# Performance work log

Hardware: AMD Instinct MI355X
Metric: run time of the kernel (lower is better)

The kernel has to match this reference:

```python
import jax, jax.numpy as jnp
from jax import lax
import numpy as np

B, C, H, W = 8, 256, 128, 128
MID, RMID = C // 2, C // 4          # heatmap-head mid, radius-head mid channels
K = 5                                # K_max centers
THR = 0.1                            # nms_threshold
SMIN, SMAX = 0.05, 0.45              # sigma clamp
BETA = 1.5                           # prior aspect ratio sigma_y/sigma_x
DMAX = 0.08                          # sigma residual max
RMIN, RMAX = 0.03, 0.40              # radius range
BNEPS = 1e-5
PI = float(np.pi)


def setup_inputs() -> dict:
    key = jax.random.key(0)
    ks = jax.random.split(key, 12)
    def n(k, shp, s):
        return jax.random.normal(k, shp, dtype=jnp.float32) * s
    return {
        'x': n(ks[0], (B, C, H, W), 1.0),
        # heatmap head: DWConv3x3 -> PW1x1 -> BN/ReLU -> Conv3x3 -> BN/ReLU -> Conv1x1(+bias=-2) -> Sigmoid
        'hm_dw': n(ks[1], (C, 1, 3, 3), 0.1),
        'hm_pw1': n(ks[2], (MID, C, 1, 1), 0.05),
        'hm_g1': jnp.ones((MID,), jnp.float32), 'hm_b1': jnp.zeros((MID,), jnp.float32),
        'hm_c3': n(ks[3], (MID, MID, 3, 3), 0.05),
        'hm_g2': jnp.ones((MID,), jnp.float32), 'hm_b2': jnp.zeros((MID,), jnp.float32),
        'hm_out_w': n(ks[4], (1, MID, 1, 1), 0.2), 'hm_out_b': jnp.full((1,), -2.0, jnp.float32),
        # radius head: DWConv3x3 -> PW1x1 -> BN/ReLU -> Conv1x1(+bias) -> Sigmoid -> [r_min, r_max]
        'r_dw': n(ks[5], (C, 1, 3, 3), 0.1),
        'r_pw1': n(ks[6], (RMID, C, 1, 1), 0.05),
        'r_g': jnp.ones((RMID,), jnp.float32), 'r_b': jnp.zeros((RMID,), jnp.float32),
        'r_out_w': n(ks[7], (1, RMID, 1, 1), 0.1), 'r_out_b': jnp.zeros((1,), jnp.float32),
        # per-center param predictor
        'log_alpha': jnp.zeros((1,), jnp.float32),
        'mlp_w1': n(ks[8], (C, C // 2), 0.05), 'mlp_b1': jnp.zeros((C // 2,), jnp.float32),
        'mlp_w2': n(ks[9], (C // 2, 4), 0.05), 'mlp_b2': jnp.zeros((4,), jnp.float32),
    }


def conv(x, w, groups=1, pad=0):
    return lax.conv_general_dilated(x, w, (1, 1), [(pad, pad), (pad, pad)],
                                    dimension_numbers=('NCHW', 'OIHW', 'NCHW'),
                                    feature_group_count=groups)


def bn(x, g, b):
    # eval-mode BatchNorm with running_mean=0, running_var=1
    s = g / np.sqrt(1.0 + BNEPS)
    return x * s[:, None, None] + b[:, None, None]


def bilinear_sample(fm, cx, cy):
    # fm: (C,H,W); cx,cy: (K,) normalized in [-1,1]; align_corners=True, border padding
    px = jnp.clip((cx + 1.0) * 0.5 * (W - 1), 0.0, W - 1)
    py = jnp.clip((cy + 1.0) * 0.5 * (H - 1), 0.0, H - 1)
    x0 = jnp.floor(px).astype(jnp.int32); x1 = jnp.minimum(x0 + 1, W - 1)
    y0 = jnp.floor(py).astype(jnp.int32); y1 = jnp.minimum(y0 + 1, H - 1)
    wx = px - x0; wy = py - y0
    v00 = fm[:, y0, x0]; v01 = fm[:, y0, x1]
    v10 = fm[:, y1, x0]; v11 = fm[:, y1, x1]          # (C,K)
    v = (1 - wy) * ((1 - wx) * v00 + wx * v01) + wy * ((1 - wx) * v10 + wx * v11)
    return v.T                                          # (K,C)


def reference(x, hm_dw, hm_pw1, hm_g1, hm_b1, hm_c3, hm_g2, hm_b2, hm_out_w, hm_out_b,
              r_dw, r_pw1, r_g, r_b, r_out_w, r_out_b,
              log_alpha, mlp_w1, mlp_b1, mlp_w2, mlp_b2):
    relu = jax.nn.relu
    # ---- heatmap head ----
    h = conv(x, hm_dw, groups=C, pad=1)
    h = conv(h, hm_pw1)
    h = relu(bn(h, hm_g1, hm_b1))
    h = conv(h, hm_c3, pad=1)
    h = relu(bn(h, hm_g2, hm_b2))
    heat = jax.nn.sigmoid(conv(h, hm_out_w) + hm_out_b[None, :, None, None])  # (B,1,H,W)
    # ---- MaxPool NMS + topk center extraction ----
    pooled = lax.reduce_window(heat, -jnp.inf, lax.max, (1, 1, 3, 3), (1, 1, 1, 1), 'SAME')
    peaks = (heat * (pooled == heat).astype(heat.dtype)).reshape(B, H * W)
    top_vals, top_idx = lax.top_k(peaks, K)             # (B,K)
    valid = (top_vals >= THR).astype(jnp.float32)
    row = (top_idx // W).astype(jnp.float32)
    col = (top_idx % W).astype(jnp.float32)
    ny = 2.0 * row / (H - 1) - 1.0
    nx = 2.0 * col / (W - 1) - 1.0
    centers = lax.stop_gradient(jnp.stack([nx, ny], -1) * valid[..., None])  # (B,K,2)
    # ---- radius map ----
    r = conv(x, r_dw, groups=C, pad=1)
    r = conv(r, r_pw1)
    r = relu(bn(r, r_g, r_b))
    rmap = RMIN + jax.nn.sigmoid(conv(r, r_out_w) + r_out_b[None, :, None, None]) * (RMAX - RMIN)
    # ---- per-center feature/radius sampling + param MLP ----
    cx, cy = centers[..., 0], centers[..., 1]
    feat = jax.vmap(bilinear_sample)(x, cx, cy)          # (B,K,C)
    r_k = jax.vmap(bilinear_sample)(rmap, cx, cy)[..., 0]  # (B,K)
    alpha = jax.nn.softplus(log_alpha)[0]
    p = relu(feat @ mlp_w1 + mlp_b1) @ mlp_w2 + mlp_b2   # (B,K,4)
    dsx = jnp.tanh(p[..., 0]) * DMAX
    dsy = jnp.tanh(p[..., 1]) * DMAX
    theta = jnp.tanh(p[..., 2]) * PI
    wgt = jax.nn.sigmoid(p[..., 3])
    sx = jnp.clip(alpha * r_k + dsx, SMIN, SMAX)
    sy = jnp.clip(alpha * r_k * BETA + dsy, SMIN, SMAX)
    # ---- rotated Gaussian mixture render ----
    yy = jnp.linspace(-1.0, 1.0, H)
    xx = jnp.linspace(-1.0, 1.0, W)
    gy, gx = jnp.meshgrid(yy, xx, indexing='ij')         # (H,W)
    dx = gx[None, None] - cx[..., None, None]            # (B,K,H,W)
    dy = gy[None, None] - cy[..., None, None]
    ct = jnp.cos(theta)[..., None, None]
    st = jnp.sin(theta)[..., None, None]
    xr = ct * dx + st * dy
    yr = -st * dx + ct * dy
    sx4 = sx[..., None, None]; sy4 = sy[..., None, None]
    G = jnp.exp(-(xr ** 2 / (2.0 * sx4 ** 2 + 1e-6) + yr ** 2 / (2.0 * sy4 ** 2 + 1e-6)))
    m = valid[..., None, None]
    mw = wgt[..., None, None] * m                         # (B,K,1,1)
    wsum = jnp.maximum(mw.sum(axis=1, keepdims=True), 1e-6)
    mix = (G * (mw / wsum) * m).sum(axis=1, keepdims=True)  # (B,1,H,W)
    attn = jax.nn.sigmoid(mix * 4.0 - 2.0)
    return jnp.concatenate([attn, heat], axis=1)          # (B,2,H,W)
```

## Files before the change

### kernel.cpp

```cpp
#include <hip/hip_runtime.h>
#include <hip/hip_bf16.h>
#include <math.h>

typedef __hip_bfloat16 bf16;
using short8 = __attribute__((ext_vector_type(8))) short;
using f32x4  = __attribute__((ext_vector_type(4))) float;

#define NB 8
#define NC 256
#define NH 128
#define NW 128
#define NHW 16384
#define MID 128
#define HP 130
#define HPP (HP*HP)

__device__ __forceinline__ float b2f(bf16 v){ return __bfloat162float(v); }
__device__ __forceinline__ bf16 f2b(float v){ return __float2bfloat16(v); }
#define BN_S 0.9999950000374997f

__global__ __launch_bounds__(256) void k_cvt(const float* __restrict__ src, bf16* __restrict__ dst, int n){
  int i = blockIdx.x*256 + threadIdx.x;
  if(i < n) dst[i] = f2b(src[i]);
}

__global__ __launch_bounds__(256) void k_trans(const float* __restrict__ src, bf16* __restrict__ dst){
  int i = blockIdx.x*256 + threadIdx.x;
  if(i >= MID*MID*9) return;
  int tau = i % 9; int c = (i/9) % MID; int m = i/(9*MID);
  dst[((size_t)tau*MID + m)*MID + c] = f2b(src[i]);
}

__global__ __launch_bounds__(256) void k_zero(bf16* __restrict__ h1p){
  int s = blockIdx.x*256 + threadIdx.x;
  const int NPLANE = NB*16;
  const int PER = 2*HP + 2*(HP-2);
  if(s >= NPLANE*PER) return;
  int plane = s / PER, j = s % PER;
  int px;
  if(j < HP)            px = j;
  else if(j < 2*HP)     px = 129*HP + (j - HP);
  else if(j < 2*HP+128) px = (j - 2*HP + 1)*HP;
  else                  px = (j - (2*HP+128) + 1)*HP + 129;
  short8 z = {0,0,0,0,0,0,0,0};
  *(short8*)((ushort*)h1p + ((size_t)plane*HPP + px)*8) = z;
}

__global__ __launch_bounds__(256) void k_dwb(const float* __restrict__ x,
                                             const float* __restrict__ w9,
                                             bf16* __restrict__ outB8){
  __shared__ float tile[8][10][136];
  int tid = threadIdx.x;
  int cg = blockIdx.y, b = blockIdx.z;
  int y0 = blockIdx.x*8;
  #pragma unroll
  for(int it=0; it<10; it++){
    int idx = it*256 + tid;
    int c = idx / 320, rem = idx % 320;
    int row = rem >> 5, col4 = rem & 31;
    int gy = y0 - 1 + row;
    float4 v = make_float4(0.f,0.f,0.f,0.f);
    if(gy >= 0 && gy < NH)
      v = *(const float4*)(x + ((size_t)(b*NC + cg*8 + c))*NHW + gy*NW + col4*4);
    *(float4*)&tile[c][row][4 + col4*4] = v;
  }
  if(tid < 160){
    int c = tid/20, rem = tid%20;
    int row = rem>>1;
    tile[c][row][(rem&1) ? 132 : 3] = 0.f;
  }
  __syncthreads();
  int row = tid >> 5;
  int t   = tid & 31;
  union { ushort u[8]; short8 v; } o[4];
  for(int c=0;c<8;c++){
    float wf[9];
    #pragma unroll
    for(int i=0;i<9;i++) wf[i] = w9[(cg*8+c)*9 + i];
    float a0=0.f, a1=0.f, a2=0.f, a3=0.f;
    #pragma unroll
    for(int dr=0;dr<3;dr++){
      float f0 = tile[c][row+dr][3 + 4*t];
      float4 v4 = *(const float4*)&tile[c][row+dr][4 + 4*t];
      float f5 = tile[c][row+dr][8 + 4*t];
      float w0 = wf[dr*3+0], w1 = wf[dr*3+1], w2 = wf[dr*3+2];
      a0 += f0*w0   + v4.x*w1 + v4.y*w2;
      a1 += v4.x*w0 + v4.y*w1 + v4.z*w2;
      a2 += v4.y*w0 + v4.z*w1 + v4.w*w2;
      a3 += v4.z*w0 + v4.w*w1 + f5*w2;
    }
    bf16 q0=f2b(a0), q1=f2b(a1), q2=f2b(a2), q3=f2b(a3);
    o[0].u[c]=*(ushort*)&q0; o[1].u[c]=*(ushort*)&q1;
    o[2].u[c]=*(ushort*)&q2; o[3].u[c]=*(ushort*)&q3;
  }
  size_t base = ((size_t)(b*32+cg))*NHW + (y0+row)*NW + 4*t;
  #pragma unroll
  for(int i=0;i<4;i++) *(short8*)(outB8 + (base+i)*8) = o[i].v;
}

template<int MT, int MODE>
__global__ __launch_bounds__(256) void k_pw(const bf16* __restrict__ in8,
                                            const bf16* __restrict__ wA,
                                            const float* __restrict__ g,
                                            const float* __restrict__ bias,
                                            const float* __restrict__ hw,
                                            const float* __restrict__ hb,
                                            bf16*  __restrict__ h1p,
                                            float* __restrict__ outMap){
  int tid = threadIdx.x;
  int bidx = blockIdx.x;
  int b = bidx >> 8;
  int p0 = (bidx & 255)*64;
  int lane = tid & 63, wave = tid >> 6;
  int n = lane & 15, quad = lane >> 4;
  size_t pix = p0 + wave*16 + n;
  const ushort* inU = (const ushort*)in8;
  const ushort* wU  = (const ushort*)wA;

  f32x4 acc[MT];
  #pragma unroll
  for(int i=0;i<MT;i++){
    #pragma unroll
    for(int r=0;r<4;r++) acc[i][r] = 0.f;
  }
  #pragma unroll
  for(int k0=0;k0<NC;k0+=32){
    short8 bfrag = *(const short8*)&inU[ (((size_t)(b*32) + (k0>>3) + quad)*NHW + pix)*8 ];
    #pragma unroll
    for(int mt=0;mt<MT;mt++){
      short8 afrag = *(const short8*)&wU[(size_t)(mt*16 + n)*NC + k0 + quad*8];
      acc[mt] = __builtin_amdgcn_mfma_f32_16x16x32_bf16(afrag, bfrag, acc[mt], 0, 0, 0);
    }
  }

  if(MODE == 0){
    int py = ((int)(pix>>7) + 1)*HP + (int)(pix&127) + 1;
    #pragma unroll
    for(int mt=0;mt<MT;mt++){
      int mg  = mt*2 + (quad>>1);
      int off = (quad&1)*4;
      union { ushort u[4]; ushort4 v; } t;
      #pragma unroll
      for(int r=0;r<4;r++){
        int m = mt*16 + quad*4 + r;
        float v = acc[mt][r]*(g[m]*BN_S) + bias[m];
        bf16 ab = f2b(fmaxf(v, 0.f));
        t.u[r] = *(ushort*)&ab;
      }
      *(ushort4*)((ushort*)h1p + (((size_t)(b*16+mg))*HPP + py)*8 + off) = t.v;
    }
  }else{
    float ph = 0.f;
    #pragma unroll
    for(int mt=0;mt<MT;mt++){
      #pragma unroll
      for(int r=0;r<4;r++){
        int m = mt*16 + quad*4 + r;
        float v = acc[mt][r]*(g[m]*BN_S) + bias[m];
        ph += fmaxf(v, 0.f) * hw[m];
      }
    }
    ph += __shfl_xor(ph, 16);
    ph += __shfl_xor(ph, 32);
    if(lane < 16){
      float sg = 1.f/(1.f + expf(-(ph + hb[0])));
      outMap[(size_t)b*NHW + pix] = 0.03f + sg*0.37f;
    }
  }
}

__global__ __launch_bounds__(256) void k_c3(const bf16* __restrict__ h1p,
                                            const bf16* __restrict__ wT,
                                            const float* __restrict__ g,
                                            const float* __restrict__ bias,
                                            const float* __restrict__ hw,
                                            const float* __restrict__ hb,
                                            float* __restrict__ heatF,
                                            float* __restrict__ out){
  int tid = threadIdx.x;
  int y = blockIdx.x, b = blockIdx.y;
  int lane = tid & 63, wave = tid >> 6;
  int n = lane & 15, quad = lane >> 4;
  const ushort* inU = (const ushort*)h1p;
  const ushort* wU  = (const ushort*)wT;
  f32x4 acc[8][2];
  #pragma unroll
  for(int i=0;i<8;i++){
    #pragma unroll
    for(int j=0;j<2;j++){
      #pragma unroll
      for(int r=0;r<4;r++) acc[i][j][r] = 0.f;
    }
  }
  int colbase = wave*32 + n;
  for(int dy=0;dy<3;dy++){
    #pragma unroll
    for(int dx=0;dx<3;dx++){
      const ushort* wtb = wU + (size_t)(dy*3+dx)*MID*MID;
      #pragma unroll
      for(int k0=0;k0<MID;k0+=32){
        size_t base = ((size_t)(b*16) + (k0>>3) + quad)*HPP + (size_t)(y+dy)*HP + colbase + dx;
        short8 b0 = *(const short8*)&inU[base*8];
        short8 b1 = *(const short8*)&inU[(base+16)*8];
        #pragma unroll
        for(int mt=0;mt<8;mt++){
          short8 a = *(const short8*)&wtb[(size_t)(mt*16 + n)*MID + k0 + quad*8];
          acc[mt][0] = __builtin_amdgcn_mfma_f32_16x16x32_bf16(a, b0, acc[mt][0], 0, 0, 0);
          acc[mt][1] = __builtin_amdgcn_mfma_f32_16x16x32_bf16(a, b1, acc[mt][1], 0, 0, 0);
        }
      }
    }
  }
  #pragma unroll
  for(int ng=0;ng<2;ng++){
    float ph = 0.f;
    #pragma unroll
    for(int mt=0;mt<8;mt++){
      #pragma unroll
      for(int r=0;r<4;r++){
        int m = mt*16 + quad*4 + r;
        float v = acc[mt][ng][r]*(g[m]*BN_S) + bias[m];
        ph += fmaxf(v, 0.f) * hw[m];
      }
    }
    ph += __shfl_xor(ph, 16);
    ph += __shfl_xor(ph, 32);
    if(lane < 16){
      int pix = y*NW + wave*32 + ng*16 + lane;
      float sg = 1.f/(1.f + expf(-(ph + hb[0])));
      heatF[(size_t)b*NHW + pix] = sg;
      out[((size_t)(b*2+1))*NHW + pix] = sg;
    }
  }
}

__global__ __launch_bounds__(256) void k_topk1(const float* __restrict__ heat,
                                               float* __restrict__ sv_g,
                                               int*   __restrict__ si_g){
  __shared__ float sv[256*5];
  __shared__ int   si[256*5];
  int blk = blockIdx.x, b = blockIdx.y, tid = threadIdx.x;
  const float* hb = heat + (size_t)b*NHW;
  float tv[5]; int ti[5];
  #pragma unroll
  for(int i=0;i<5;i++){ tv[i] = -1.f; ti[i] = 0x7fffffff; }
  for(int s=0;s<2;s++){
    int p = blk*512 + s*256 + tid;
    int y = p >> 7, x = p & 127;
    float v = hb[p];
    float mx = v;
    for(int dy=-1;dy<=1;dy++){
      int yy = y+dy; if(yy<0||yy>=NH) continue;
      for(int dx=-1;dx<=1;dx++){
        int xc = x+dx; if(xc<0||xc>=NW) continue;
        mx = fmaxf(mx, hb[yy*NW+xc]);
      }
    }
    float pv = (v == mx) ? v : 0.f;
    #pragma unroll
    for(int j=0;j<5;j++){
      if(pv > tv[j] || (pv == tv[j] && p < ti[j])){
        for(int q=4;q>j;q--){ tv[q]=tv[q-1]; ti[q]=ti[q-1]; }
        tv[j] = pv; ti[j] = p;
        break;
      }
    }
  }
  #pragma unroll
  for(int i=0;i<5;i++){ sv[tid*5+i] = tv[i]; si[tid*5+i] = ti[i]; }
  __syncthreads();
  if(tid < 64){
    float mv[5]; int mi[5];
    #pragma unroll
    for(int i=0;i<5;i++){ mv[i] = -1.f; mi[i] = 0x7fffffff; }
    for(int s=0;s<4;s++){
      int t2 = tid + s*64;
      for(int i=0;i<5;i++){
        float pv = sv[t2*5+i]; int pi = si[t2*5+i];
        for(int j=0;j<5;j++){
          if(pv > mv[j] || (pv == mv[j] && pi < mi[j])){
            for(int q=4;q>j;q--){ mv[q]=mv[q-1]; mi[q]=mi[q-1]; }
            mv[j] = pv; mi[j] = pi;
            break;
          }
        }
      }
    }
    for(int i=0;i<5;i++){ sv[tid*5+i] = mv[i]; si[tid*5+i] = mi[i]; }
  }
  __syncthreads();
  if(tid == 0){
    float fv[5]; int fi[5];
    #pragma unroll
    for(int i=0;i<5;i++){ fv[i] = -1.f; fi[i] = 0x7fffffff; }
    for(int t2=0;t2<64;t2++){
      for(int i=0;i<5;i++){
        float pv = sv[t2*5+i]; int pi = si[t2*5+i];
        for(int j=0;j<5;j++){
          if(pv > fv[j] || (pv == fv[j] && pi < fi[j])){
            for(int q=4;q>j;q--){ fv[q]=fv[q-1]; fi[q]=fi[q-1]; }
            fv[j] = pv; fi[j] = pi;
            break;
          }
        }
      }
    }
    for(int i=0;i<5;i++){
      sv_g[(b*32 + blk)*5 + i] = fv[i];
      si_g[(b*32 + blk)*5 + i] = fi[i];
    }
  }
}

__global__ __launch_bounds__(256) void k_topk2(const float* __restrict__ sv_g,
                                               const int*   __restrict__ si_g,
                                               float* __restrict__ centers){
  __shared__ float cv[160];
  __shared__ int   ci[160];
  int b = blockIdx.x, tid = threadIdx.x;
  if(tid < 160){ cv[tid] = sv_g[b*160 + tid]; ci[tid] = si_g[b*160 + tid]; }
  __syncthreads();
  if(tid < 160){
    float v = cv[tid]; int idx = ci[tid];
    int rank = 0;
    for(int j=0;j<160;j++){
      float vj = cv[j]; int ij = ci[j];
      rank += (vj > v || (vj == v && ij < idx)) ? 1 : 0;
    }
    if(rank < 5){
      float valid = (v >= 0.1f) ? 1.f : 0.f;
      float row = (float)(idx >> 7);
      float col = (float)(idx & 127);
      float ny = 2.f*row/127.f - 1.f;
      float nx = 2.f*col/127.f - 1.f;
      float* cp = centers + (b*5+rank)*4;
      cp[0] = nx*valid; cp[1] = ny*valid; cp[2] = v; cp[3] = valid;
    }
  }
}

__global__ __launch_bounds__(256) void k_params(const float* __restrict__ x,
                                                const float* __restrict__ rmap,
                                                const float* __restrict__ centers,
                                                const float* __restrict__ w1,
                                                const float* __restrict__ b1,
                                                const float* __restrict__ w2,
                                                const float* __restrict__ b2,
                                                const float* __restrict__ log_alpha,
                                                float* __restrict__ params){
  __shared__ float feat[NC];
  __shared__ float hmid[128];
  __shared__ float pp[4];
  int bk = blockIdx.x;
  int b = bk/5;
  int tid = threadIdx.x;
  float cx = centers[bk*4+0];
  float cy = centers[bk*4+1];
  float valid = centers[bk*4+3];
  float px = fminf(fmaxf((cx+1.f)*0.5f*(NW-1), 0.f), (float)(NW-1));
  float py = fminf(fmaxf((cy+1.f)*0.5f*(NH-1), 0.f), (float)(NH-1));
  int x0 = (int)floorf(px); int x1 = min(x0+1, NW-1);
  int y0 = (int)floorf(py); int y1 = min(y0+1, NH-1);
  float wx = px - (float)x0, wy = py - (float)y0;
  {
    const float* xb = x + ((size_t)b*NC + tid)*NHW;
    float v00 = xb[y0*NW+x0], v01 = xb[y0*NW+x1];
    float v10 = xb[y1*NW+x0], v11 = xb[y1*NW+x1];
    feat[tid] = (1.f-wy)*((1.f-wx)*v00 + wx*v01) + wy*((1.f-wx)*v10 + wx*v11);
  }
  __syncthreads();
  if(tid < 128){
    float a = b1[tid];
    for(int c=0;c<NC;c++) a += feat[c]*w1[c*128+tid];
    hmid[tid] = fmaxf(a, 0.f);
  }
  __syncthreads();
  if(tid < 4){
    float a = b2[tid];
    for(int j=0;j<128;j++) a += hmid[j]*w2[j*4+tid];
    pp[tid] = a;
  }
  __syncthreads();
  if(tid == 0){
    const float* rb = rmap + (size_t)b*NHW;
    float r00 = rb[y0*NW+x0], r01 = rb[y0*NW+x1];
    float r10 = rb[y1*NW+x0], r11 = rb[y1*NW+x1];
    float rk = (1.f-wy)*((1.f-wx)*r00 + wx*r01) + wy*((1.f-wx)*r10 + wx*r11);
    float la = log_alpha[0];
    float alpha = logf(1.f + expf(la));
    float dsx = tanhf(pp[0])*0.08f;
    float dsy = tanhf(pp[1])*0.08f;
    float theta = tanhf(pp[2])*3.14159265358979323846f;
    float wgt = 1.f/(1.f + expf(-pp[3]));
    float sx = fminf(fmaxf(alpha*rk + dsx, 0.05f), 0.45f);
    float sy = fminf(fmaxf(alpha*rk*1.5f + dsy, 0.05f), 0.45f);
    float* P = params + bk*8;
    P[0] = cx; P[1] = cy;
    P[2] = cosf(theta); P[3] = sinf(theta);
    P[4] = 1.f/(2.f*sx*sx + 1e-6f);
    P[5] = 1.f/(2.f*sy*sy + 1e-6f);
    P[6] = wgt*valid; P[7] = valid;
  }
}

__global__ __launch_bounds__(256) void k_attn(const float* __restrict__ params,
                                              float* __restrict__ out){
  int tid = threadIdx.x;
  int p = blockIdx.x*256 + tid;
  int b = blockIdx.y;
  int y = p >> 7, x = p & 127;
  float gx = -1.f + 2.f*(float)x/127.f;
  float gy = -1.f + 2.f*(float)y/127.f;
  const float* Pb = params + b*40;
  float wsum = 0.f;
  #pragma unroll
  for(int k=0;k<5;k++) wsum += Pb[k*8+6];
  wsum = fmaxf(wsum, 1e-6f);
  float mix = 0.f;
  #pragma unroll
  for(int k=0;k<5;k++){
    const float* P = Pb + k*8;
    float dx = gx - P[0], dy = gy - P[1];
    float xr =  P[2]*dx + P[3]*dy;
    float yr = -P[3]*dx + P[2]*dy;
    float e = __expf(-(xr*xr*P[4] + yr*yr*P[5]));
    mix += e * (P[6]/wsum);
  }
  float attn = 1.f/(1.f + __expf(-(4.f*mix - 2.f)));
  out[((size_t)(b*2))*NHW + p] = attn;
}

extern "C" void kernel_launch(void* const* d_in, const int* in_sizes, int n_in,
                              void* d_out, int out_size, void* d_ws, size_t ws_size,
                              hipStream_t stream){
  const float* x        = (const float*)d_in[0];
  const float* hm_dw    = (const float*)d_in[1];
  const float* hm_pw1   = (const float*)d_in[2];
  const float* hm_g1    = (const float*)d_in[3];
  const float* hm_b1    = (const float*)d_in[4];
  const float* hm_c3    = (const float*)d_in[5];
  const float* hm_g2    = (const float*)d_in[6];
  const float* hm_b2    = (const float*)d_in[7];
  const float* hm_out_w = (const float*)d_in[8];
  const float* hm_out_b = (const float*)d_in[9];
  const float* r_dw     = (const float*)d_in[10];
  const float* r_pw1    = (const float*)d_in[11];
  const float* r_g      = (const float*)d_in[12];
  const float* r_b      = (const float*)d_in[13];
  const float* r_out_w  = (const float*)d_in[14];
  const float* r_out_b  = (const float*)d_in[15];
  const float* log_alpha= (const float*)d_in[16];
  const float* mlp_w1   = (const float*)d_in[17];
  const float* mlp_b1   = (const float*)d_in[18];
  const float* mlp_w2   = (const float*)d_in[19];
  const float* mlp_b2   = (const float*)d_in[20];
  float* out = (float*)d_out;

  char* ws = (char*)d_ws;
  bf16*  dwX     = (bf16*)ws;
  bf16*  h1p     = (bf16*)(ws + 67108864);
  float* heatF   = (float*)(ws + 101720064);
  float* rmapF   = (float*)(ws + 102244352);
  bf16*  wT      = (bf16*)(ws + 102768640);
  bf16*  wPW1h   = (bf16*)(ws + 103063552);
  bf16*  wPW1r   = (bf16*)(ws + 103129088);
  float* tsv     = (float*)(ws + 103161856);
  int*   tsi     = (int*)  (ws + 103166976);
  float* centers = (float*)(ws + 103172096);
  float* params  = (float*)(ws + 103172736);

  k_cvt  <<<dim3(128), dim3(256), 0, stream>>>(hm_pw1, wPW1h, 128*256);
  k_cvt  <<<dim3(64),  dim3(256), 0, stream>>>(r_pw1,  wPW1r, 64*256);
  k_trans<<<dim3(576), dim3(256), 0, stream>>>(hm_c3, wT);
  k_zero <<<dim3((NB*16*516 + 255)/256), dim3(256), 0, stream>>>(h1p);

  k_dwb<<<dim3(16, 32, NB), dim3(256), 0, stream>>>(x, r_dw, dwX);
  k_pw<4,1><<<dim3(2048), dim3(256), 0, stream>>>(dwX, wPW1r, r_g, r_b,
                                                  r_out_w, r_out_b,
                                                  (bf16*)nullptr, rmapF);
  k_dwb<<<dim3(16, 32, NB), dim3(256), 0, stream>>>(x, hm_dw, dwX);
  k_pw<8,0><<<dim3(2048), dim3(256), 0, stream>>>(dwX, wPW1h, hm_g1, hm_b1,
                                                  (const float*)nullptr, (const float*)nullptr,
                                                  h1p, (float*)nullptr);
  k_c3<<<dim3(128, NB), dim3(256), 0, stream>>>(h1p, wT, hm_g2, hm_b2, hm_out_w, hm_out_b, heatF, out);
  k_topk1<<<dim3(32, NB), dim3(256), 0, stream>>>(heatF, tsv, tsi);
  k_topk2<<<dim3(NB), dim3(256), 0, stream>>>(tsv, tsi, centers);
  k_params<<<dim3(NB*5), dim3(256), 0, stream>>>(x, rmapF, centers, mlp_w1, mlp_b1, mlp_w2, mlp_b2, log_alpha, params);
  k_attn<<<dim3(64, NB), dim3(256), 0, stream>>>(params, out);
}
```

Before: 704.7 us.

## Fuse both depthwise convs, retile pointwise GEMMs, split 3x3 conv over output channels

Adds a fused depthwise kernel that reads the input tile once and writes both the heatmap and radius depthwise outputs, when the workspace is large enough. The pointwise MFMA kernel is retiled to 128 pixels by 64 output channels per block, so each B fragment is reused across two pixel groups. The 3x3 conv is split over two output-channel halves through a grid z dimension, writing partial logits that a new small kernel sums and passes through the sigmoid. This is meant to cut reads of x, lower register pressure and raise occupancy. It costs an extra launch and a partial-sum buffer, and the fused path needs a second 64MB workspace buffer.

```diff
diff --git a/kernel.cpp b/kernel.cpp
--- a/kernel.cpp
+++ b/kernel.cpp
@@ -98,7 +98,72 @@
   for(int i=0;i<4;i++) *(short8*)(outB8 + (base+i)*8) = o[i].v;
 }
 
-template<int MT, int MODE>
+__global__ __launch_bounds__(256) void k_dwb2(const float* __restrict__ x,
+                                              const float* __restrict__ wA9,
+                                              const float* __restrict__ wB9,
+                                              bf16* __restrict__ outA,
+                                              bf16* __restrict__ outB){
+  __shared__ float tile[8][10][136];
+  int tid = threadIdx.x;
+  int cg = blockIdx.y, b = blockIdx.z;
+  int y0 = blockIdx.x*8;
+  #pragma unroll
+  for(int it=0; it<10; it++){
+    int idx = it*256 + tid;
+    int c = idx / 320, rem = idx % 320;
+    int row = rem >> 5, col4 = rem & 31;
+    int gy = y0 - 1 + row;
+    float4 v = make_float4(0.f,0.f,0.f,0.f);
+    if(gy >= 0 && gy < NH)
+      v = *(const float4*)(x + ((size_t)(b*NC + cg*8 + c))*NHW + gy*NW + col4*4);
+    *(float4*)&tile[c][row][4 + col4*4] = v;
+  }
+  if(tid < 160){
+    int c = tid/20, rem = tid%20;
+    int row = rem>>1;
+    tile[c][row][(rem&1) ? 132 : 3] = 0.f;
+  }
+  __syncthreads();
+  int row = tid >> 5;
+  int t   = tid & 31;
+  union { ushort u[8]; short8 v; } oA[4], oB[4];
+  for(int c=0;c<8;c++){
+    float wfA[9], wfB[9];
+    #pragma unroll
+    for(int i=0;i<9;i++){ wfA[i] = wA9[(cg*8+c)*9 + i]; wfB[i] = wB9[(cg*8+c)*9 + i]; }
+    float aA0=0.f,aA1=0.f,aA2=0.f,aA3=0.f;
+    float aB0=0.f,aB1=0.f,aB2=0.f,aB3=0.f;
+    #pragma unroll
+    for(int dr=0;dr<3;dr++){
+      float f0 = tile[c][row+dr][3 + 4*t];
+      float4 v4 = *(const float4*)&tile[c][row+dr][4 + 4*t];
+      float f5 = tile[c][row+dr][8 + 4*t];
+      float wa0=wfA[dr*3+0], wa1=wfA[dr*3+1], wa2=wfA[dr*3+2];
+      float wb0=wfB[dr*3+0], wb1=wfB[dr*3+1], wb2=wfB[dr*3+2];
+      aA0 += f0*wa0   + v4.x*wa1 + v4.y*wa2;
+      aA1 += v4.x*wa0 + v4.y*wa1 + v4.z*wa2;
+      aA2 += v4.y*wa0 + v4.z*wa1 + v4.w*wa2;
+      aA3 += v4.z*wa0 + v4.w*wa1 + f5*wa2;
+      aB0 += f0*wb0   + v4.x*wb1 + v4.y*wb2;
+      aB1 += v4.x*wb0 + v4.y*wb1 + v4.z*wb2;
+      aB2 += v4.y*wb0 + v4.z*wb1 + v4.w*wb2;
+      aB3 += v4.z*wb0 + v4.w*wb1 + f5*wb2;
+    }
+    bf16 q;
+    q=f2b(aA0); oA[0].u[c]=*(ushort*)&q;  q=f2b(aA1); oA[1].u[c]=*(ushort*)&q;
+    q=f2b(aA2); oA[2].u[c]=*(ushort*)&q;  q=f2b(aA3); oA[3].u[c]=*(ushort*)&q;
+    q=f2b(aB0); oB[0].u[c]=*(ushort*)&q;  q=f2b(aB1); oB[1].u[c]=*(ushort*)&q;
+    q=f2b(aB2); oB[2].u[c]=*(ushort*)&q;  q=f2b(aB3); oB[3].u[c]=*(ushort*)&q;
+  }
+  size_t base = ((size_t)(b*32+cg))*NHW + (y0+row)*NW + 4*t;
+  #pragma unroll
+  for(int i=0;i<4;i++){
+    *(short8*)(outA + (base+i)*8) = oA[i].v;
+    *(short8*)(outB + (base+i)*8) = oB[i].v;
+  }
+}
+
+template<int MODE>
 __global__ __launch_bounds__(256) void k_pw(const bf16* __restrict__ in8,
                                             const bf16* __restrict__ wA,
                                             const float* __restrict__ g,
@@ -109,62 +174,76 @@
                                             float* __restrict__ outMap){
   int tid = threadIdx.x;
   int bidx = blockIdx.x;
-  int b = bidx >> 8;
-  int p0 = (bidx & 255)*64;
+  int b = bidx >> 7;
+  int p0 = (bidx & 127)*128;
+  int Moff = blockIdx.y*64;
   int lane = tid & 63, wave = tid >> 6;
   int n = lane & 15, quad = lane >> 4;
-  size_t pix = p0 + wave*16 + n;
+  size_t pix0 = p0 + wave*32 + n;
   const ushort* inU = (const ushort*)in8;
   const ushort* wU  = (const ushort*)wA;
 
-  f32x4 acc[MT];
-  #pragma unroll
-  for(int i=0;i<MT;i++){
-    #pragma unroll
-    for(int r=0;r<4;r++) acc[i][r] = 0.f;
-  }
+  f32x4 acc[4][2];
+  #pragma unroll
+  for(int i=0;i<4;i++)
+    #pragma unroll
+    for(int j=0;j<2;j++)
+      #pragma unroll
+      for(int r=0;r<4;r++) acc[i][j][r] = 0.f;
+
   #pragma unroll
   for(int k0=0;k0<NC;k0+=32){
-    short8 bfrag = *(const short8*)&inU[ (((size_t)(b*32) + (k0>>3) + quad)*NHW + pix)*8 ];
-    #pragma unroll
-    for(int mt=0;mt<MT;mt++){
-      short8 afrag = *(const short8*)&wU[(size_t)(mt*16 + n)*NC + k0 + quad*8];
-      acc[mt] = __builtin_amdgcn_mfma_f32_16x16x32_bf16(afrag, bfrag, acc[mt], 0, 0, 0);
+    size_t gb = ((size_t)(b*32) + (k0>>3) + quad)*NHW;
+    short8 b0 = *(const short8*)&inU[(gb + pix0)*8];
+    short8 b1 = *(const short8*)&inU[(gb + pix0 + 16)*8];
+    #pragma unroll
+    for(int mt=0;mt<4;mt++){
+      short8 a = *(const short8*)&wU[(size_t)(Moff + mt*16 + n)*NC + k0 + quad*8];
+      acc[mt][0] = __builtin_amdgcn_mfma_f32_16x16x32_bf16(a, b0, acc[mt][0], 0, 0, 0);
+      acc[mt][1] = __builtin_amdgcn_mfma_f32_16x16x32_bf16(a, b1, acc[mt][1], 0, 0, 0);
     }
   }
 
   if(MODE == 0){
-    int py = ((int)(pix>>7) + 1)*HP + (int)(pix&127) + 1;
-    #pragma unroll
-    for(int mt=0;mt<MT;mt++){
-      int mg  = mt*2 + (quad>>1);
-      int off = (quad&1)*4;
-      union { ushort u[4]; ushort4 v; } t;
+    #pragma unroll
+    for(int ng=0;ng<2;ng++){
+      size_t pix = pix0 + ng*16;
+      int py = ((int)(pix>>7) + 1)*HP + (int)(pix&127) + 1;
       #pragma unroll
-      for(int r=0;r<4;r++){
-        int m = mt*16 + quad*4 + r;
-        float v = acc[mt][r]*(g[m]*BN_S) + bias[m];
-        bf16 ab = f2b(fmaxf(v, 0.f));
-        t.u[r] = *(ushort*)&ab;
-      }
-      *(ushort4*)((ushort*)h1p + (((size_t)(b*16+mg))*HPP + py)*8 + off) = t.v;
+      for(int mt=0;mt<4;mt++){
+        int mg  = (Moff>>3) + mt*2 + (quad>>1);
+        int off = (quad&1)*4;
+        union { ushort u[4]; ushort4 v; } t;
+        #pragma unroll
+        for(int r=0;r<4;r++){
+          int m = Moff + mt*16 + quad*4 + r;
+          float v = acc[mt][ng][r]*(g[m]*BN_S) + bias[m];
+          bf16 ab = f2b(fmaxf(v, 0.f));
+          t.u[r] = *(ushort*)&ab;
+        }
+        *(ushort4*)((ushort*)h1p + (((size_t)(b*16+mg))*HPP + py)*8 + off) = t.v;
+      }
     }
   }else{
-    float ph = 0.f;
-    #pragma unroll
-    for(int mt=0;mt<MT;mt++){
+    #pragma unroll
+    for(int ng=0;ng<2;ng++){
+      float ph = 0.f;
       #pragma unroll
-      for(int r=0;r<4;r++){
-        int m = mt*16 + quad*4 + r;
-        float v = acc[mt][r]*(g[m]*BN_S) + bias[m];
-        ph += fmaxf(v, 0.f) * hw[m];
-      }
-    }
-    ph += __shfl_xor(ph, 16);
-    ph += __shfl_xor(ph, 32);
-    if(lane < 16){
-      float sg = 1.f/(1.f + expf(-(ph + hb[0])));
-      outMap[(size_t)b*NHW + pix] = 0.03f + sg*0.37f;
+      for(int mt=0;mt<4;mt++){
+        #pragma unroll
+        for(int r=0;r<4;r++){
+          int m = mt*16 + quad*4 + r;
+          float v = acc[mt][ng][r]*(g[m]*BN_S) + bias[m];
+          ph += fmaxf(v, 0.f) * hw[m];
+        }
+      }
+      ph += __shfl_xor(ph, 16);
+      ph += __shfl_xor(ph, 32);
+      if(lane < 16){
+        int pix = p0 + wave*32 + ng*16 + lane;
+        float sg = 1.f/(1.f + expf(-(ph + hb[0])));
+        outMap[(size_t)b*NHW + pix] = 0.03f + sg*0.37f;
+      }
     }
   }
 }
@@ -174,36 +253,34 @@
                                             const float* __restrict__ g,
                                             const float* __restrict__ bias,
                                             const float* __restrict__ hw,
-                                            const float* __restrict__ hb,
-                                            float* __restrict__ heatF,
-                                            float* __restrict__ out){
+                                            float* __restrict__ partialH){
   int tid = threadIdx.x;
   int y = blockIdx.x, b = blockIdx.y;
+  int Moff = blockIdx.z*64;
   int lane = tid & 63, wave = tid >> 6;
   int n = lane & 15, quad = lane >> 4;
   const ushort* inU = (const ushort*)h1p;
   const ushort* wU  = (const ushort*)wT;
-  f32x4 acc[8][2];
-  #pragma unroll
-  for(int i=0;i<8;i++){
-    #pragma unroll
-    for(int j=0;j<2;j++){
+  f32x4 acc[4][2];
+  #pragma unroll
+  for(int i=0;i<4;i++)
+    #pragma unroll
+    for(int j=0;j<2;j++)
       #pragma unroll
       for(int r=0;r<4;r++) acc[i][j][r] = 0.f;
-    }
-  }
+
   int colbase = wave*32 + n;
   for(int dy=0;dy<3;dy++){
     #pragma unroll
     for(int dx=0;dx<3;dx++){
-      const ushort* wtb = wU + (size_t)(dy*3+dx)*MID*MID;
+      const ushort* wtb = wU + (size_t)(dy*3+dx)*MID*MID + (size_t)Moff*MID;
       #pragma unroll
       for(int k0=0;k0<MID;k0+=32){
         size_t base = ((size_t)(b*16) + (k0>>3) + quad)*HPP + (size_t)(y+dy)*HP + colbase + dx;
         short8 b0 = *(const short8*)&inU[base*8];
         short8 b1 = *(const short8*)&inU[(base+16)*8];
         #pragma unroll
-        for(int mt=0;mt<8;mt++){
+        for(int mt=0;mt<4;mt++){
           short8 a = *(const short8*)&wtb[(size_t)(mt*16 + n)*MID + k0 + quad*8];
           acc[mt][0] = __builtin_amdgcn_mfma_f32_16x16x32_bf16(a, b0, acc[mt][0], 0, 0, 0);
           acc[mt][1] = __builtin_amdgcn_mfma_f32_16x16x32_bf16(a, b1, acc[mt][1], 0, 0, 0);
@@ -215,10 +292,10 @@
   for(int ng=0;ng<2;ng++){
     float ph = 0.f;
     #pragma unroll
-    for(int mt=0;mt<8;mt++){
+    for(int mt=0;mt<4;mt++){
       #pragma unroll
       for(int r=0;r<4;r++){
-        int m = mt*16 + quad*4 + r;
+        int m = Moff + mt*16 + quad*4 + r;
         float v = acc[mt][ng][r]*(g[m]*BN_S) + bias[m];
         ph += fmaxf(v, 0.f) * hw[m];
       }
@@ -227,11 +304,21 @@
     ph += __shfl_xor(ph, 32);
     if(lane < 16){
       int pix = y*NW + wave*32 + ng*16 + lane;
-      float sg = 1.f/(1.f + expf(-(ph + hb[0])));
-      heatF[(size_t)b*NHW + pix] = sg;
-      out[((size_t)(b*2+1))*NHW + pix] = sg;
-    }
-  }
+      partialH[((size_t)blockIdx.z*NB + b)*NHW + pix] = ph;
+    }
+  }
+}
+
+__global__ __launch_bounds__(256) void k_heat(const float* __restrict__ partialH,
+                                              const float* __restrict__ hb,
+                                              float* __restrict__ heatF,
+                                              float* __restrict__ out){
+  int p = blockIdx.x*256 + threadIdx.x;
+  int b = blockIdx.y;
+  float logit = partialH[(size_t)b*NHW + p] + partialH[(size_t)(NB + b)*NHW + p] + hb[0];
+  float sg = 1.f/(1.f + expf(-logit));
+  heatF[(size_t)b*NHW + p] = sg;
+  out[((size_t)(b*2+1))*NHW + p] = sg;
 }
 
 __global__ __launch_bounds__(256) void k_topk1(const float* __restrict__ heat,
@@ -456,33 +543,49 @@
   const float* mlp_b2   = (const float*)d_in[20];
   float* out = (float*)d_out;
 
+  const size_t SZ_DW  = 67108864;
+  const size_t SZ_H1P = 34611200;
   char* ws = (char*)d_ws;
-  bf16*  dwX     = (bf16*)ws;
-  bf16*  h1p     = (bf16*)(ws + 67108864);
-  float* heatF   = (float*)(ws + 101720064);
-  float* rmapF   = (float*)(ws + 102244352);
-  bf16*  wT      = (bf16*)(ws + 102768640);
-  bf16*  wPW1h   = (bf16*)(ws + 103063552);
-  bf16*  wPW1r   = (bf16*)(ws + 103129088);
-  float* tsv     = (float*)(ws + 103161856);
-  int*   tsi     = (int*)  (ws + 103166976);
-  float* centers = (float*)(ws + 103172096);
-  float* params  = (float*)(ws + 103172736);
+
+  bool big = ws_size >= (2*SZ_DW + SZ_H1P + 2*1024*1024);
+  bf16* dwXh = (bf16*)ws;
+  bf16* dwXr = big ? (bf16*)(ws + SZ_DW) : dwXh;
+  size_t off = (big ? 2*SZ_DW : SZ_DW);
+  bf16*  h1p   = (bf16*)(ws + off);               off += SZ_H1P;
+  float* heatF = (float*)(ws + off);              off += 524288;
+  float* rmapF = (float*)(ws + off);              off += 524288;
+  bf16*  wT    = (bf16*)(ws + off);               off += 294912;
+  bf16*  wPW1h = (bf16*)(ws + off);               off += 65536;
+  bf16*  wPW1r = (bf16*)(ws + off);               off += 32768;
+  float* tsv   = (float*)(ws + off);              off += 5120;
+  int*   tsi   = (int*)(ws + off);                off += 5120;
+  float* centers = (float*)(ws + off);            off += 640;
+  float* params  = (float*)(ws + off);            off += 1280;
+  float* partialH = (float*)ws;
 
   k_cvt  <<<dim3(128), dim3(256), 0, stream>>>(hm_pw1, wPW1h, 128*256);
   k_cvt  <<<dim3(64),  dim3(256), 0, stream>>>(r_pw1,  wPW1r, 64*256);
   k_trans<<<dim3(576), dim3(256), 0, stream>>>(hm_c3, wT);
   k_zero <<<dim3((NB*16*516 + 255)/256), dim3(256), 0, stream>>>(h1p);
 
-  k_dwb<<<dim3(16, 32, NB), dim3(256), 0, stream>>>(x, r_dw, dwX);
-  k_pw<4,1><<<dim3(2048), dim3(256), 0, stream>>>(dwX, wPW1r, r_g, r_b,
-                                                  r_out_w, r_out_b,
-                                                  (bf16*)nullptr, rmapF);
-  k_dwb<<<dim3(16, 32, NB), dim3(256), 0, stream>>>(x, hm_dw, dwX);
-  k_pw<8,0><<<dim3(2048), dim3(256), 0, stream>>>(dwX, wPW1h, hm_g1, hm_b1,
-                                                  (const float*)nullptr, (const float*)nullptr,
-                                                  h1p, (float*)nullptr);
-  k_c3<<<dim3(128, NB), dim3(256), 0, stream>>>(h1p, wT, hm_g2, hm_b2, hm_out_w, hm_out_b, heatF, out);
+  if(big){
+    k_dwb2<<<dim3(16, 32, NB), dim3(256), 0, stream>>>(x, hm_dw, r_dw, dwXh, dwXr);
+    k_pw<1><<<dim3(1024, 1), dim3(256), 0, stream>>>(dwXr, wPW1r, r_g, r_b, r_out_w, r_out_b,
+                                                     (bf16*)nullptr, rmapF);
+    k_pw<0><<<dim3(1024, 2), dim3(256), 0, stream>>>(dwXh, wPW1h, hm_g1, hm_b1,
+                                                     (const float*)nullptr, (const float*)nullptr,
+                                                     h1p, (float*)nullptr);
+  }else{
+    k_dwb<<<dim3(16, 32, NB), dim3(256), 0, stream>>>(x, r_dw, dwXr);
+    k_pw<1><<<dim3(1024, 1), dim3(256), 0, stream>>>(dwXr, wPW1r, r_g, r_b, r_out_w, r_out_b,
+                                                     (bf16*)nullptr, rmapF);
+    k_dwb<<<dim3(16, 32, NB), dim3(256), 0, stream>>>(x, hm_dw, dwXh);
+    k_pw<0><<<dim3(1024, 2), dim3(256), 0, stream>>>(dwXh, wPW1h, hm_g1, hm_b1,
+                                                     (const float*)nullptr, (const float*)nullptr,
+                                                     h1p, (float*)nullptr);
+  }
+  k_c3<<<dim3(128, NB, 2), dim3(256), 0, stream>>>(h1p, wT, hm_g2, hm_b2, hm_out_w, partialH);
+  k_heat<<<dim3(64, NB), dim3(256), 0, stream>>>(partialH, hm_out_b, heatF, out);
   k_topk1<<<dim3(32, NB), dim3(256), 0, stream>>>(heatF, tsv, tsi);
   k_topk2<<<dim3(NB), dim3(256), 0, stream>>>(tsv, tsi, centers);
   k_params<<<dim3(NB*5), dim3(256), 0, stream>>>(x, rmapF, centers, mlp_w1, mlp_b1, mlp_w2, mlp_b2, log_alpha, params);
```

New measurement: 638.5 us. 1.1x faster.
